# Kernel optimization log

Measured on AMD Instinct MI355X. Metric: run time of the kernel, lower is better.

The kernel has to match this reference:

```python
import jax, jax.numpy as jnp
import numpy as np

EMBED = 256
HEADS = 8
LEVELS = 4
POINTS = 4
HD = EMBED // HEADS  # 32


def _bilinear_sample(v, grid):
    """torch.F.grid_sample(mode='bilinear', padding_mode='zeros', align_corners=False).
    v: (B, C, H, W); grid: (B, Q, P, 2) with xy coords in [-1, 1].
    Returns (B, C, Q, P).
    """
    B, C, H, W = v.shape
    x = (grid[..., 0] + 1.0) * (W * 0.5) - 0.5
    y = (grid[..., 1] + 1.0) * (H * 0.5) - 0.5
    x0f = jnp.floor(x)
    y0f = jnp.floor(y)
    wx = x - x0f
    wy = y - y0f
    x0 = x0f.astype(jnp.int32)
    y0 = y0f.astype(jnp.int32)
    vf = v.reshape(B, C, H * W)

    def corner(xi, yi, w):
        valid = (xi >= 0) & (xi < W) & (yi >= 0) & (yi < H)
        idx = jnp.clip(yi, 0, H - 1) * W + jnp.clip(xi, 0, W - 1)  # (B, Q, P)
        g = jax.vmap(lambda vb, ib: jnp.take(vb, ib, axis=1))(vf, idx.reshape(B, -1))
        g = g.reshape(B, C, idx.shape[1], idx.shape[2])  # (B, C, Q, P)
        return g * (w * valid.astype(v.dtype))[:, None]

    return (corner(x0, y0, (1 - wx) * (1 - wy))
            + corner(x0 + 1, y0, wx * (1 - wy))
            + corner(x0, y0 + 1, (1 - wx) * wy)
            + corner(x0 + 1, y0 + 1, wx * wy))


def setup_inputs() -> dict:
    key = jax.random.key(0)
    ks = jax.random.split(key, 16)
    N, Q, D = 2, 8192, EMBED
    inp = {
        'query': jax.random.normal(ks[0], (N, Q, D), jnp.float32),
        'feat0': jax.random.normal(ks[1], (N, D, 64, 64), jnp.float32),
        'feat1': jax.random.normal(ks[2], (N, D, 32, 32), jnp.float32),
        'feat2': jax.random.normal(ks[3], (N, D, 16, 16), jnp.float32),
        'feat3': jax.random.normal(ks[4], (N, D, 8, 8), jnp.float32),
        'reference_points': jax.random.uniform(ks[5], (N, Q, 2), jnp.float32),
        # params stored as (in, out); equivalent math to torch Linear's x @ W.T + b
        'W_off': jax.random.normal(ks[6], (D, HEADS * LEVELS * POINTS * 2), jnp.float32) * 0.01,
        'b_off': jax.random.normal(ks[7], (HEADS * LEVELS * POINTS * 2,), jnp.float32) * 0.01,
        'W_attn': jax.random.normal(ks[8], (D, HEADS * LEVELS * POINTS), jnp.float32) * 0.02,
        'b_attn': jax.random.normal(ks[9], (HEADS * LEVELS * POINTS,), jnp.float32) * 0.02,
        'W_val': jax.random.normal(ks[10], (D, D), jnp.float32) * (1.0 / np.sqrt(D)),
        'b_val': jnp.zeros((D,), jnp.float32),
        'W_out': jax.random.normal(ks[11], (D, D), jnp.float32) * (1.0 / np.sqrt(D)),
        'b_out': jnp.zeros((D,), jnp.float32),
    }
    return inp


def reference(query, feat0, feat1, feat2, feat3, reference_points,
              W_off, b_off, W_attn, b_attn, W_val, b_val, W_out, b_out):
    feats = [feat0, feat1, feat2, feat3]
    N, Q, D = query.shape
    # offset / attention-weight projections
    off = (query @ W_off + b_off).reshape(N, Q, HEADS, LEVELS, POINTS, 2)
    attn = (query @ W_attn + b_attn).reshape(N, Q, HEADS, LEVELS, POINTS)
    # reference points (N,Q,2) -> (N,Q,L,2)
    ref = jnp.broadcast_to(reference_points[:, :, None, :], (N, Q, LEVELS, 2))
    # value projection (1x1 conv) per level, split heads -> (N*H, hd, H_l, W_l)
    vals = [(jnp.einsum('bchw,cd->bdhw', f, W_val) + b_val[None, :, None, None])
            .reshape(N * HEADS, HD, f.shape[2], f.shape[3]) for f in feats]
    # flatten batch*heads
    off = off.transpose(0, 2, 1, 3, 4, 5).reshape(N * HEADS, Q, LEVELS, POINTS, 2)
    attn = attn.transpose(0, 2, 1, 3, 4).reshape(N * HEADS, Q, LEVELS, POINTS)
    refh = jnp.broadcast_to(ref[:, None], (N, HEADS, Q, LEVELS, 2)).reshape(N * HEADS, Q, LEVELS, 2)
    loc = refh[:, :, :, None, :] + off                 # (NH, Q, L, P, 2) in [0,1]
    grid = 2.0 * loc - 1.0                             # [-1, 1]
    # per-level bilinear sampling -> (NH, hd, Q, L, P)
    sampled = jnp.stack([_bilinear_sample(vals[l], grid[:, :, l]) for l in range(LEVELS)], axis=-2)
    # softmax over levels*points
    aw = jax.nn.softmax(attn.reshape(N * HEADS, Q, LEVELS * POINTS), axis=-1)
    aw = jnp.nan_to_num(aw).reshape(N * HEADS, Q, LEVELS, POINTS)
    out = jnp.einsum('bcqlp,bqlp->bcq', sampled, aw)   # (NH, hd, Q)
    out = out.reshape(N, HEADS, HD, Q).transpose(0, 3, 1, 2).reshape(N, Q, D)
    return out @ W_out + b_out
```

## Files before the change

### kernel.cpp

```cpp
#include <hip/hip_runtime.h>
#include <math.h>

#define NB 2
#define QN 8192
#define DIM 256
#define S_TOT 5440

typedef unsigned int uint32;
typedef _Float16 f16;
typedef __attribute__((ext_vector_type(8))) _Float16 h8;
typedef __attribute__((ext_vector_type(2))) _Float16 h2;
typedef __attribute__((ext_vector_type(4))) float f32x4;


__global__ __launch_bounds__(256) void prep_kernel(
    const float* __restrict__ q,
    const float* __restrict__ f0, const float* __restrict__ f1,
    const float* __restrict__ f2, const float* __restrict__ f3,
    const float* __restrict__ W_off, const float* __restrict__ W_attn,
    const float* __restrict__ W_val, const float* __restrict__ W_out,
    f16* __restrict__ qf, f16* __restrict__ featT_f,
    f16* __restrict__ Wcat_f, f16* __restrict__ Wval_f, f16* __restrict__ Wout_f) {
  const int t = blockIdx.x, y = blockIdx.y, tid = threadIdx.x;

  if (t < 128) {
    const int row0 = (t * 8 + y) * 16;
    const int s_l = tid >> 4, c8 = tid & 15;
    const float* src = q + (size_t)(row0 + s_l) * 256;
#pragma unroll
    for (int cc = 0; cc < 2; ++cc) {
      const int c8c = c8 + cc * 16;
      const float4 u0 = *(const float4*)(src + c8c * 8);
      const float4 u1 = *(const float4*)(src + c8c * 8 + 4);
      h8 hv = {(f16)u0.x, (f16)u0.y, (f16)u0.z, (f16)u0.w,
               (f16)u1.x, (f16)u1.y, (f16)u1.z, (f16)u1.w};
      *(h8*)(qf + ((size_t)(row0 >> 4) * 32 + c8c) * 128 + s_l * 8) = hv;
    }
    return;
  }

  __shared__ float tile[32][33];
  const int tx = tid & 31, ty = tid >> 5;
  const float* src;
  f16* dst;
  int S, tb, s_base = 0;

  if (t < 468) {
    const int tt0 = t - 128;
    const int b = (tt0 >= 170) ? 1 : 0;
    const int tt = tt0 - 170 * b;
    int soff;
    if (tt < 128)      { src = f0; S = 4096; soff = 0;    tb = tt; }
    else if (tt < 160) { src = f1; S = 1024; soff = 4096; tb = tt - 128; }
    else if (tt < 168) { src = f2; S = 256;  soff = 5120; tb = tt - 160; }
    else               { src = f3; S = 64;   soff = 5376; tb = tt - 168; }
    src += (size_t)b * 256 * S;
    dst = featT_f;
    s_base = b * S_TOT + soff;
  } else {
    const int tw = t - 468;
    if (tw < 8)       { src = W_off;  dst = Wcat_f; S = 256; tb = tw;      s_base = 0; }
    else if (tw < 12) { src = W_attn; dst = Wcat_f; S = 128; tb = tw - 8;  s_base = 256; }
    else if (tw < 20) { src = W_val;  dst = Wval_f; S = 256; tb = tw - 12; s_base = 0; }
    else              { src = W_out;  dst = Wout_f; S = 256; tb = tw - 20; s_base = 0; }
  }
  const int s0 = tb * 32, c0 = y * 32;

#pragma unroll
  for (int j = 0; j < 4; ++j) {
    const int c = c0 + ty + j * 8;
    tile[ty + j * 8][tx] = src[(size_t)c * S + s0 + tx];
  }
  __syncthreads();

  if (tid < 128) {
    const int s_l = tid >> 2, c8l = tid & 3;
    const int Sg = s_base + s0 + s_l;
    const int c8 = (c0 >> 3) + c8l;
    h8 v;
#pragma unroll
    for (int j = 0; j < 8; ++j) v[j] = (f16)tile[c8l * 8 + j][s_l];
    *(h8*)(dst + ((size_t)(Sg >> 4) * 32 + c8) * 128 + (Sg & 15) * 8) = v;
  }
}

__global__ __launch_bounds__(256) void gemm_fused_kernel(
    const f16* __restrict__ qf, const f16* __restrict__ featT_f,
    const f16* __restrict__ Wcat_f, const f16* __restrict__ Wval_f,
    const float* __restrict__ b_val, const float* __restrict__ b_off,
    const float* __restrict__ b_attn,
    f16* __restrict__ vals, f16* __restrict__ offb, f16* __restrict__ attnb) {
  const int t = blockIdx.x;
  const int tid = threadIdx.x;
  const int lane = tid & 63, wid = tid >> 6;
  const int l15 = lane & 15, l4 = lane >> 4;

  if (t < 340) {
    const int g0 = t * 2;
    f32x4 acc[2][4] = {};
#pragma unroll
    for (int ks = 0; ks < 8; ++ks) {
      const int s2 = ks * 4 + l4;
      h8 a[2], b[4];
#pragma unroll
      for (int m = 0; m < 2; ++m)
        a[m] = *(const h8*)(featT_f + ((size_t)(g0 + m) * 32 + s2) * 128 + l15 * 8);
#pragma unroll
      for (int n = 0; n < 4; ++n)
        b[n] = *(const h8*)(Wval_f + ((size_t)(wid * 4 + n) * 32 + s2) * 128 + l15 * 8);
#pragma unroll
      for (int m = 0; m < 2; ++m)
#pragma unroll
        for (int n = 0; n < 4; ++n)
          acc[m][n] = __builtin_amdgcn_mfma_f32_16x16x32_f16(a[m], b[n], acc[m][n], 0, 0, 0);
    }
#pragma unroll
    for (int m = 0; m < 2; ++m)
#pragma unroll
      for (int n = 0; n < 4; ++n)
#pragma unroll
        for (int r = 0; r < 4; ++r) {
          const size_t rw = (size_t)t * 32 + m * 16 + l4 * 4 + r;
          const int col = wid * 64 + n * 16 + l15;
          vals[rw * 256 + col] = (f16)(acc[m][n][r] + b_val[col]);
        }
  } else {
    const int t2 = t - 340;
    const int g0 = t2 * 2;
    f32x4 acc[2][6] = {};
#pragma unroll
    for (int ks = 0; ks < 8; ++ks) {
      const int s2 = ks * 4 + l4;
      h8 a[2], b[6];
#pragma unroll
      for (int m = 0; m < 2; ++m)
        a[m] = *(const h8*)(qf + ((size_t)(g0 + m) * 32 + s2) * 128 + l15 * 8);
#pragma unroll
      for (int n = 0; n < 6; ++n)
        b[n] = *(const h8*)(Wcat_f + ((size_t)(wid * 6 + n) * 32 + s2) * 128 + l15 * 8);
#pragma unroll
      for (int m = 0; m < 2; ++m)
#pragma unroll
        for (int n = 0; n < 6; ++n)
          acc[m][n] = __builtin_amdgcn_mfma_f32_16x16x32_f16(a[m], b[n], acc[m][n], 0, 0, 0);
    }
#pragma unroll
    for (int m = 0; m < 2; ++m)
#pragma unroll
      for (int n = 0; n < 6; ++n)
#pragma unroll
        for (int r = 0; r < 4; ++r) {
          const size_t rw = (size_t)t2 * 32 + m * 16 + l4 * 4 + r;
          const int col = wid * 96 + n * 16 + l15;
          const float v = acc[m][n][r];
          if (col < 256)
            offb[rw * 256 + col] = (f16)(v + b_off[col]);
          else
            attnb[rw * 128 + (col - 256)] = (f16)(v + b_attn[col - 256]);
        }
  }
}

__global__ __launch_bounds__(256) void gemm_out_kernel(
    const f16* __restrict__ A, const f16* __restrict__ Bt,
    const float* __restrict__ bias, float* __restrict__ out) {
  const int tid = threadIdx.x;
  const int lane = tid & 63, wid = tid >> 6;
  const int l15 = lane & 15, l4 = lane >> 4;
  const int g0 = blockIdx.x * 2;

  f32x4 acc[2][4] = {};
#pragma unroll
  for (int ks = 0; ks < 8; ++ks) {
    const int s2 = ks * 4 + l4;
    h8 a[2], b[4];
#pragma unroll
    for (int m = 0; m < 2; ++m)
      a[m] = *(const h8*)(A + ((size_t)(g0 + m) * 32 + s2) * 128 + l15 * 8);
#pragma unroll
    for (int n = 0; n < 4; ++n)
      b[n] = *(const h8*)(Bt + ((size_t)(wid * 4 + n) * 32 + s2) * 128 + l15 * 8);
#pragma unroll
    for (int m = 0; m < 2; ++m)
#pragma unroll
      for (int n = 0; n < 4; ++n)
        acc[m][n] = __builtin_amdgcn_mfma_f32_16x16x32_f16(a[m], b[n], acc[m][n], 0, 0, 0);
  }

#pragma unroll
  for (int m = 0; m < 2; ++m)
#pragma unroll
    for (int n = 0; n < 4; ++n)
#pragma unroll
      for (int r = 0; r < 4; ++r) {
        const size_t rw = (size_t)blockIdx.x * 32 + m * 16 + l4 * 4 + r;
        const int col = wid * 64 + n * 16 + l15;
        out[rw * 256 + col] = acc[m][n][r] + bias[col];
      }
}

__global__ __launch_bounds__(256) void sample_kernel(
    const f16* __restrict__ vals, const f16* __restrict__ offb,
    const f16* __restrict__ attnb, const float* __restrict__ refp,
    f16* __restrict__ samp_f) {
  const int tid = threadIdx.x;
  const int g = tid & 15;
  const int grp = tid >> 4;
  const int h = grp & 7;
  const int half = tid >> 7;
  const int bq = blockIdx.x * 2 + half;
  const int b = bq >> 13;

  __shared__ float4 wts[16][17];
  __shared__ int4 idxs[16][17];

  const float rx = refp[(size_t)bq * 2 + 0];
  const float ry = refp[(size_t)bq * 2 + 1];

  float logit = (float)attnb[(size_t)bq * 128 + h * 16 + g];
  float m = logit;
#pragma unroll
  for (int mask = 1; mask < 16; mask <<= 1)
    m = fmaxf(m, __shfl_xor(m, mask, 16));
  const float e = __expf(logit - m);
  float ssum = e;
#pragma unroll
  for (int mask = 1; mask < 16; mask <<= 1)
    ssum += __shfl_xor(ssum, mask, 16);
  const float aw = e / ssum;

  const h2 ov = *(const h2*)(offb + (size_t)bq * 256 + h * 32 + g * 2);
  const int l = g >> 2;
  const int Wl = 64 >> l;
  const int loff = (l == 0) ? 0 : (l == 1) ? 4096 : (l == 2) ? 5120 : 5376;

  const float px = (rx + (float)ov[0]) * (float)Wl - 0.5f;
  const float py = (ry + (float)ov[1]) * (float)Wl - 0.5f;
  const float fx = floorf(px), fy = floorf(py);
  const float wx = px - fx, wy = py - fy;
  const int x0 = (int)fx, y0 = (int)fy;
  const int x1 = x0 + 1, y1 = y0 + 1;
  const float vx0 = (x0 >= 0 && x0 < Wl) ? 1.f : 0.f;
  const float vx1 = (x1 >= 0 && x1 < Wl) ? 1.f : 0.f;
  const float vy0 = (y0 >= 0 && y0 < Wl) ? 1.f : 0.f;
  const float vy1 = (y1 >= 0 && y1 < Wl) ? 1.f : 0.f;
  const int cx0 = min(max(x0, 0), Wl - 1), cx1 = min(max(x1, 0), Wl - 1);
  const int cy0 = min(max(y0, 0), Wl - 1), cy1 = min(max(y1, 0), Wl - 1);
  const int base = b * S_TOT + loff;
  idxs[grp][g] = make_int4((base + cy0 * Wl + cx0) * 512,
                           (base + cy0 * Wl + cx1) * 512,
                           (base + cy1 * Wl + cx0) * 512,
                           (base + cy1 * Wl + cx1) * 512);
  wts[grp][g] = make_float4(aw * (1.f - wx) * (1.f - wy) * vx0 * vy0,
                            aw * wx * (1.f - wy) * vx1 * vy0,
                            aw * (1.f - wx) * wy * vx0 * vy1,
                            aw * wx * wy * vx1 * vy1);
  __syncthreads();

  const int c4 = g & 3, pc = g >> 2;
  const char* vb = (const char*)vals + (h * 64 + c4 * 16);

  float wv[16];
  int ids[16];
#pragma unroll
  for (int pt = 0; pt < 16; ++pt) {
    wv[pt] = ((const float*)&wts[grp][pt])[pc];
    ids[pt] = ((const int*)&idxs[grp][pt])[pc];
  }
  h8 vv[16];
#pragma unroll
  for (int pt = 0; pt < 16; ++pt) vv[pt] = *(const h8*)(vb + ids[pt]);

  float a[8] = {};
#pragma unroll
  for (int pt = 0; pt < 16; ++pt) {
#pragma unroll
    for (int k = 0; k < 8; ++k) a[k] = fmaf((float)vv[pt][k], wv[pt], a[k]);
  }
#pragma unroll
  for (int k = 0; k < 8; ++k) {
    a[k] += __shfl_xor(a[k], 4);
    a[k] += __shfl_xor(a[k], 8);
  }
  if (pc == 0) {
    h8 r;
#pragma unroll
    for (int k = 0; k < 8; ++k) r[k] = (f16)a[k];
    *(h8*)(samp_f + ((size_t)(bq >> 4) * 32 + h * 4 + c4) * 128 + (bq & 15) * 8) = r;
  }
}

extern "C" void kernel_launch(void* const* d_in, const int* in_sizes, int n_in,
                              void* d_out, int out_size, void* d_ws, size_t ws_size,
                              hipStream_t stream) {
  const float* query = (const float*)d_in[0];
  const float* feat[4] = {(const float*)d_in[1], (const float*)d_in[2],
                          (const float*)d_in[3], (const float*)d_in[4]};
  const float* refp  = (const float*)d_in[5];
  const float* W_off = (const float*)d_in[6];
  const float* b_off = (const float*)d_in[7];
  const float* W_attn = (const float*)d_in[8];
  const float* b_attn = (const float*)d_in[9];
  const float* W_val = (const float*)d_in[10];
  const float* b_val = (const float*)d_in[11];
  const float* W_out = (const float*)d_in[12];
  const float* b_out = (const float*)d_in[13];
  float* out = (float*)d_out;

  f16* ws = (f16*)d_ws;
  f16* vals    = ws;
  f16* offb    = vals + (size_t)NB * S_TOT * 256;
  f16* attnb   = offb + (size_t)NB * QN * 256;
  f16* qf      = attnb + (size_t)NB * QN * 128;
  f16* samp_f  = qf;
  f16* featT_f = qf + (size_t)NB * QN * 256;
  f16* Wcat_f  = featT_f + (size_t)NB * S_TOT * 256;
  f16* Wval_f  = Wcat_f + 384 * 256;
  f16* Wout_f  = Wval_f + 256 * 256;

  prep_kernel<<<dim3(496, 8), 256, 0, stream>>>(
      query, feat[0], feat[1], feat[2], feat[3],
      W_off, W_attn, W_val, W_out, qf, featT_f, Wcat_f, Wval_f, Wout_f);

  gemm_fused_kernel<<<340 + 512, 256, 0, stream>>>(
      qf, featT_f, Wcat_f, Wval_f, b_val, b_off, b_attn, vals, offb, attnb);

  sample_kernel<<<(NB * QN) / 2, 256, 0, stream>>>(vals, offb, attnb, refp, samp_f);

  gemm_out_kernel<<<(NB * QN) / 32, 256, 0, stream>>>(samp_f, Wout_f, b_out, out);
}
```

Baseline: 69.34 us.

## Process one query per block in sampler, splitting points across thread pairs

The sampling kernel now handles one query per 256-thread block instead of two. Half the threads compute softmax weights and corner indices into shared memory. All threads then gather and accumulate, each covering 8 of the 16 sample points, with an extra cross-lane shuffle to combine the two halves. This doubles the grid size and halves per-thread gather and register load to raise parallelism and memory-level concurrency, at the cost of idle threads during setup, an extra shuffle, and more block launches.

```diff
diff --git a/kernel.cpp b/kernel.cpp
--- a/kernel.cpp
+++ b/kernel.cpp
@@ -204,85 +204,88 @@
     const f16* __restrict__ attnb, const float* __restrict__ refp,
     f16* __restrict__ samp_f) {
   const int tid = threadIdx.x;
-  const int g = tid & 15;
-  const int grp = tid >> 4;
-  const int h = grp & 7;
-  const int half = tid >> 7;
-  const int bq = blockIdx.x * 2 + half;
+  const int bq = blockIdx.x;
   const int b = bq >> 13;
 
-  __shared__ float4 wts[16][17];
-  __shared__ int4 idxs[16][17];
-
-  const float rx = refp[(size_t)bq * 2 + 0];
-  const float ry = refp[(size_t)bq * 2 + 1];
-
-  float logit = (float)attnb[(size_t)bq * 128 + h * 16 + g];
-  float m = logit;
-#pragma unroll
-  for (int mask = 1; mask < 16; mask <<= 1)
-    m = fmaxf(m, __shfl_xor(m, mask, 16));
-  const float e = __expf(logit - m);
-  float ssum = e;
-#pragma unroll
-  for (int mask = 1; mask < 16; mask <<= 1)
-    ssum += __shfl_xor(ssum, mask, 16);
-  const float aw = e / ssum;
-
-  const h2 ov = *(const h2*)(offb + (size_t)bq * 256 + h * 32 + g * 2);
-  const int l = g >> 2;
-  const int Wl = 64 >> l;
-  const int loff = (l == 0) ? 0 : (l == 1) ? 4096 : (l == 2) ? 5120 : 5376;
-
-  const float px = (rx + (float)ov[0]) * (float)Wl - 0.5f;
-  const float py = (ry + (float)ov[1]) * (float)Wl - 0.5f;
-  const float fx = floorf(px), fy = floorf(py);
-  const float wx = px - fx, wy = py - fy;
-  const int x0 = (int)fx, y0 = (int)fy;
-  const int x1 = x0 + 1, y1 = y0 + 1;
-  const float vx0 = (x0 >= 0 && x0 < Wl) ? 1.f : 0.f;
-  const float vx1 = (x1 >= 0 && x1 < Wl) ? 1.f : 0.f;
-  const float vy0 = (y0 >= 0 && y0 < Wl) ? 1.f : 0.f;
-  const float vy1 = (y1 >= 0 && y1 < Wl) ? 1.f : 0.f;
-  const int cx0 = min(max(x0, 0), Wl - 1), cx1 = min(max(x1, 0), Wl - 1);
-  const int cy0 = min(max(y0, 0), Wl - 1), cy1 = min(max(y1, 0), Wl - 1);
-  const int base = b * S_TOT + loff;
-  idxs[grp][g] = make_int4((base + cy0 * Wl + cx0) * 512,
-                           (base + cy0 * Wl + cx1) * 512,
-                           (base + cy1 * Wl + cx0) * 512,
-                           (base + cy1 * Wl + cx1) * 512);
-  wts[grp][g] = make_float4(aw * (1.f - wx) * (1.f - wy) * vx0 * vy0,
-                            aw * wx * (1.f - wy) * vx1 * vy0,
-                            aw * (1.f - wx) * wy * vx0 * vy1,
-                            aw * wx * wy * vx1 * vy1);
+  __shared__ float4 wts[8][16];
+  __shared__ int4 idxs[8][16];
+
+  if (tid < 128) {
+    const int h = tid >> 4, pt = tid & 15;
+    const float rx = refp[(size_t)bq * 2 + 0];
+    const float ry = refp[(size_t)bq * 2 + 1];
+
+    float logit = (float)attnb[(size_t)bq * 128 + tid];
+    float m = logit;
+#pragma unroll
+    for (int mask = 1; mask < 16; mask <<= 1)
+      m = fmaxf(m, __shfl_xor(m, mask, 16));
+    const float e = __expf(logit - m);
+    float ssum = e;
+#pragma unroll
+    for (int mask = 1; mask < 16; mask <<= 1)
+      ssum += __shfl_xor(ssum, mask, 16);
+    const float aw = e / ssum;
+
+    const h2 ov = *(const h2*)(offb + (size_t)bq * 256 + h * 32 + pt * 2);
+    const int l = pt >> 2;
+    const int Wl = 64 >> l;
+    const int loff = (l == 0) ? 0 : (l == 1) ? 4096 : (l == 2) ? 5120 : 5376;
+
+    const float px = (rx + (float)ov[0]) * (float)Wl - 0.5f;
+    const float py = (ry + (float)ov[1]) * (float)Wl - 0.5f;
+    const float fx = floorf(px), fy = floorf(py);
+    const float wx = px - fx, wy = py - fy;
+    const int x0 = (int)fx, y0 = (int)fy;
+    const int x1 = x0 + 1, y1 = y0 + 1;
+    const float vx0 = (x0 >= 0 && x0 < Wl) ? 1.f : 0.f;
+    const float vx1 = (x1 >= 0 && x1 < Wl) ? 1.f : 0.f;
+    const float vy0 = (y0 >= 0 && y0 < Wl) ? 1.f : 0.f;
+    const float vy1 = (y1 >= 0 && y1 < Wl) ? 1.f : 0.f;
+    const int cx0 = min(max(x0, 0), Wl - 1), cx1 = min(max(x1, 0), Wl - 1);
+    const int cy0 = min(max(y0, 0), Wl - 1), cy1 = min(max(y1, 0), Wl - 1);
+    const int base = b * S_TOT + loff;
+    idxs[h][pt] = make_int4((base + cy0 * Wl + cx0) * 512,
+                            (base + cy0 * Wl + cx1) * 512,
+                            (base + cy1 * Wl + cx0) * 512,
+                            (base + cy1 * Wl + cx1) * 512);
+    wts[h][pt] = make_float4(aw * (1.f - wx) * (1.f - wy) * vx0 * vy0,
+                             aw * wx * (1.f - wy) * vx1 * vy0,
+                             aw * (1.f - wx) * wy * vx0 * vy1,
+                             aw * wx * wy * vx1 * vy1);
+  }
   __syncthreads();
 
+  const int grp = tid >> 4, g = tid & 15;
+  const int h = grp >> 1, ph = grp & 1;
   const int c4 = g & 3, pc = g >> 2;
   const char* vb = (const char*)vals + (h * 64 + c4 * 16);
 
-  float wv[16];
-  int ids[16];
-#pragma unroll
-  for (int pt = 0; pt < 16; ++pt) {
-    wv[pt] = ((const float*)&wts[grp][pt])[pc];
-    ids[pt] = ((const int*)&idxs[grp][pt])[pc];
-  }
-  h8 vv[16];
-#pragma unroll
-  for (int pt = 0; pt < 16; ++pt) vv[pt] = *(const h8*)(vb + ids[pt]);
+  float wv[8];
+  int ids[8];
+#pragma unroll
+  for (int i = 0; i < 8; ++i) {
+    const int pt = ph * 8 + i;
+    wv[i] = ((const float*)&wts[h][pt])[pc];
+    ids[i] = ((const int*)&idxs[h][pt])[pc];
+  }
+  h8 vv[8];
+#pragma unroll
+  for (int i = 0; i < 8; ++i) vv[i] = *(const h8*)(vb + ids[i]);
 
   float a[8] = {};
 #pragma unroll
-  for (int pt = 0; pt < 16; ++pt) {
-#pragma unroll
-    for (int k = 0; k < 8; ++k) a[k] = fmaf((float)vv[pt][k], wv[pt], a[k]);
+  for (int i = 0; i < 8; ++i) {
+#pragma unroll
+    for (int k = 0; k < 8; ++k) a[k] = fmaf((float)vv[i][k], wv[i], a[k]);
   }
 #pragma unroll
   for (int k = 0; k < 8; ++k) {
     a[k] += __shfl_xor(a[k], 4);
     a[k] += __shfl_xor(a[k], 8);
-  }
-  if (pc == 0) {
+    a[k] += __shfl_xor(a[k], 16);
+  }
+  if (pc == 0 && ph == 0) {
     h8 r;
 #pragma unroll
     for (int k = 0; k < 8; ++k) r[k] = (f16)a[k];
@@ -325,7 +328,7 @@
   gemm_fused_kernel<<<340 + 512, 256, 0, stream>>>(
       qf, featT_f, Wcat_f, Wval_f, b_val, b_off, b_attn, vals, offb, attnb);
 
-  sample_kernel<<<(NB * QN) / 2, 256, 0, stream>>>(vals, offb, attnb, refp, samp_f);
+  sample_kernel<<<NB * QN, 256, 0, stream>>>(vals, offb, attnb, refp, samp_f);
 
   gemm_out_kernel<<<(NB * QN) / 32, 256, 0, stream>>>(samp_f, Wout_f, b_out, out);
 }
```

Result: slower. 75.26 us (+8.5%).
